# Optimization experiments

Hardware: AMD Instinct MI355X
Metric: run time of the kernel (lower is better)

Reference implementation:

```python
import jax, jax.numpy as jnp
import numpy as np

T, B, E, H = 1024, 4, 1024, 16
Dh = E // H
NEG_INF = float('-inf')


def setup_inputs() -> dict:
    key = jax.random.key(0)
    k1, k2, k3, k4 = jax.random.split(key, 4)
    return {
        'fwd_x': jax.random.normal(k1, (T, B, E), jnp.float32),
        'bwd_x': jax.random.normal(k2, (T, B, E), jnp.float32),
        'in_proj_weight': jax.random.normal(k3, (3 * E, E), jnp.float32) * 0.02,
        'in_proj_bias': jnp.zeros((3 * E,), jnp.float32),
        'out_w': jax.random.normal(k4, (E, E), jnp.float32) * 0.02,
        'out_b': jnp.zeros((E,), jnp.float32),
    }


def reference(fwd_x, bwd_x, in_proj_weight, in_proj_bias, out_w, out_b):
    t, b, e = fwd_x.shape
    s = 2 * t
    dtype = fwd_x.dtype
    zeros = jnp.zeros((1, b, e), dtype)
    # padded_fwd_x[0:t] -> [0, fwd_x[:-1]]; padded_bwd_x[1:t+1] -> [bwd_x[1:], 0]
    q_in = jnp.concatenate([zeros, fwd_x[:-1]], 0) + jnp.concatenate([bwd_x[1:], zeros], 0)
    kv = jnp.concatenate([fwd_x, bwd_x], 0)  # [s, b, e]

    wq, wk, wv = in_proj_weight[:e], in_proj_weight[e:2 * e], in_proj_weight[2 * e:]
    bq, bk, bv = in_proj_bias[:e], in_proj_bias[e:2 * e], in_proj_bias[2 * e:]
    q = (q_in @ wq.T + bq).reshape(t, b, H, Dh)
    k = (kv @ wk.T + bk).reshape(s, b, H, Dh)
    v = (kv @ wv.T + bv).reshape(s, b, H, Dh)

    # NOTE: original module never applies self.scaling in forward -- keep unscaled.
    attn_weights = jnp.einsum('tbhd,sbhd->bhts', q, k)  # [b, H, t, s]

    # mask_curr_state=True: allowed keys are j < i (fwd half) or j > i + t (bwd half)
    i = jnp.arange(t)[:, None]
    j = jnp.arange(s)[None, :]
    allowed = (j >= i + t + 1) | (j <= i - 1)
    mask_bias = jnp.where(allowed, 0.0, NEG_INF).astype(dtype)
    attn_weights = attn_weights + mask_bias[None, None]

    probs = jax.nn.softmax(attn_weights.astype(jnp.float32), axis=-1).astype(dtype)

    attn = jnp.einsum('bhts,sbhd->tbhd', probs, v).reshape(t, b, e)
    attn = attn @ out_w.T + out_b
    avg_weights = probs.mean(axis=1)  # [b, t, s]
    return attn, avg_weights
```

## Files before the change

### kernel.cpp

```cpp
#include <hip/hip_runtime.h>

typedef unsigned short u16;
typedef __attribute__((ext_vector_type(8))) short short8;
typedef __attribute__((ext_vector_type(4))) float f32x4;

#define SM_SHIFT2 34.6246800f
#if defined(__has_builtin)
#if __has_builtin(__builtin_amdgcn_exp2f)
#define EXP2(x) __builtin_amdgcn_exp2f(x)
#else
#define EXP2(x) __expf((x) * 0.6931471805599453f)
#endif
#else
#define EXP2(x) __expf((x) * 0.6931471805599453f)
#endif

__device__ __forceinline__ u16 f2b(float f) {
  unsigned u = __float_as_uint(f);
  unsigned r = (u + 0x7FFFu + ((u >> 16) & 1u)) >> 16;
  return (u16)r;
}

__device__ __forceinline__ void gload16(const u16* g, u16* l) {
  __builtin_amdgcn_global_load_lds((const __attribute__((address_space(1))) void*)g,
                                   (__attribute__((address_space(3))) void*)l, 16, 0, 0);
}

__device__ __forceinline__ void cast4(const float* __restrict__ src,
                                      u16* __restrict__ dst, int gid) {
  float4 v = *(const float4*)(src + (gid << 2));
  ushort4 o; o.x = f2b(v.x); o.y = f2b(v.y); o.z = f2b(v.z); o.w = f2b(v.w);
  *(ushort4*)(dst + (gid << 2)) = o;
}

__global__ __launch_bounds__(256) void prep_all(const float* __restrict__ fwd,
                                                const float* __restrict__ bwd,
                                                const float* __restrict__ w_in,
                                                const float* __restrict__ w_out,
                                                u16* __restrict__ qin,
                                                u16* __restrict__ kvf,
                                                u16* __restrict__ kvb,
                                                u16* __restrict__ wbf,
                                                u16* __restrict__ wobf,
                                                float* __restrict__ out_avg) {
  const int blk = blockIdx.x, tid = threadIdx.x;
  if (blk < 4096) {
    int gid = blk * 256 + tid;
    int n = gid >> 8;
    int e4 = (gid & 255) << 2;
    int t = n >> 2, b = n & 3;
    float4 acc = make_float4(0.f, 0.f, 0.f, 0.f);
    if (t > 0) {
      float4 v = *(const float4*)(fwd + (((t - 1) * 4 + b) << 10) + e4);
      acc.x += v.x; acc.y += v.y; acc.z += v.z; acc.w += v.w;
    }
    if (t < 1023) {
      float4 v = *(const float4*)(bwd + (((t + 1) * 4 + b) << 10) + e4);
      acc.x += v.x; acc.y += v.y; acc.z += v.z; acc.w += v.w;
    }
    ushort4 o; o.x = f2b(acc.x); o.y = f2b(acc.y); o.z = f2b(acc.z); o.w = f2b(acc.w);
    *(ushort4*)(qin + (n << 10) + e4) = o;
  } else if (blk < 8192) {
    cast4(fwd, kvf, (blk - 4096) * 256 + tid);
  } else if (blk < 12288) {
    cast4(bwd, kvb, (blk - 8192) * 256 + tid);
  } else if (blk < 15360) {
    cast4(w_in, wbf, (blk - 12288) * 256 + tid);
  } else if (blk < 16384) {
    cast4(w_out, wobf, (blk - 15360) * 256 + tid);
  } else {
    int z = blk - 16384;
    int mi = z % 15, bt2 = z / 15;
    int tb2 = bt2 & 15, b2 = bt2 >> 4;
    int s0z = (tb2 + 1 + mi) << 6, t0z = tb2 << 6;
    float* ob = out_avg + (size_t)b2 * 2097152 + (size_t)t0z * 2048 + s0z;
    float4 zz = make_float4(0.f, 0.f, 0.f, 0.f);
#pragma unroll
    for (int it = 0; it < 4; ++it) {
      int idx = it * 256 + tid;
      int rr = idx >> 4, c4 = (idx & 15) << 2;
      *(float4*)&ob[rr * 2048 + c4] = zz;
    }
  }
}

__global__ __launch_bounds__(512, 2) void gemm_kv256(const u16* __restrict__ A,
                                                     const u16* __restrict__ W,
                                                     const float* __restrict__ bias,
                                                     u16* __restrict__ outK,
                                                     u16* __restrict__ outV) {
  __shared__ u16 SH[65536];
  const int x = blockIdx.x & 7, local = blockIdx.x >> 3;
  const int mt = x * 4 + (local & 3);
  const int nt = local >> 2;
  const int m0 = mt << 8, n0 = nt << 8;
  const int tid = threadIdx.x;
  const int lane = tid & 63, wid = tid >> 6;
  const int wm = (wid >> 2) << 7;
  const int wn = (wid & 3) << 6;
  const int lr = lane & 15, lg = lane >> 4;
  const int scol = (lane & 7) << 3;
  const int swc = ((lane & 7) ^ (lane >> 3)) << 3;
  f32x4 acc[8][4] = {};
  auto At = [&](int buf) { return SH + buf * 16384; };
  auto Wt = [&](int buf) { return SH + 32768 + buf * 16384; };
  auto stage = [&](int buf, int k0) {
    u16* a = At(buf); u16* w = Wt(buf);
#pragma unroll
    for (int it = 0; it < 4; it++) {
      int row = (it * 8 + wid) * 8 + (lane >> 3);
      gload16(&A[(size_t)(m0 + row) * 1024 + k0 + swc], &a[row * 64 + scol]);
      gload16(&W[(size_t)(n0 + row) * 1024 + k0 + swc], &w[row * 64 + scol]);
    }
  };
  auto compute = [&](int buf) {
    const u16* a = At(buf); const u16* w = Wt(buf);
#pragma unroll
    for (int kk = 0; kk < 64; kk += 32) {
      int co = (((kk >> 3) + lg) ^ (lr & 7)) << 3;
      short8 af[8], bf[4];
#pragma unroll
      for (int i = 0; i < 8; i++)
        af[i] = *(const short8*)&a[(wm + i * 16 + lr) * 64 + co];
#pragma unroll
      for (int j = 0; j < 4; j++)
        bf[j] = *(const short8*)&w[(wn + j * 16 + lr) * 64 + co];
#pragma unroll
      for (int i = 0; i < 8; i++)
#pragma unroll
        for (int j = 0; j < 4; j++)
          acc[i][j] = __builtin_amdgcn_mfma_f32_16x16x32_bf16(af[i], bf[j], acc[i][j], 0, 0, 0);
    }
  };
  stage(0, 0);
  __syncthreads();
  for (int step = 0; step < 16; ++step) {
    const int cur = step & 1;
    if (step < 15) stage(cur ^ 1, (step + 1) << 6);
    compute(cur);
    __syncthreads();
  }
  u16* C = SH;
#pragma unroll
  for (int i = 0; i < 8; i++) {
#pragma unroll
    for (int j = 0; j < 4; j++) {
      int n = wn + j * 16 + lr;
      float bv = bias[n0 + n];
      int np = n ^ (lg << 4);
#pragma unroll
      for (int r = 0; r < 4; r++) {
        int m = wm + i * 16 + lg * 4 + r;
        C[m * 256 + np] = f2b(acc[i][j][r] + bv);
      }
    }
  }
  __syncthreads();
  const bool isK = (n0 < 1024);
  u16* ob = isK ? outK : outV;
  const int hbase = isK ? (n0 >> 6) : ((n0 - 1024) >> 6);
  const int ts0 = m0 >> 2;
  const int ts = tid >> 3, c8d = tid & 7;
#pragma unroll
  for (int k = 0; k < 16; ++k) {
    int tb = k >> 2, hh = k & 3;
    int m = ts * 4 + tb;
    int c8 = (hh * 8 + c8d) ^ ((ts & 3) << 1);
    uint4 val = *(const uint4*)&C[m * 256 + c8 * 8];
    size_t off = ((size_t)(tb * 16 + hbase + hh) * 2048 + ts0 + ts) * 64 + c8d * 8;
    *(uint4*)&ob[off] = val;
  }
}

template <int MODE, int MTX>
__global__ __launch_bounds__(256) void gemm_bt(const u16* __restrict__ A,
                                               const u16* __restrict__ W,
                                               const float* __restrict__ bias,
                                               void* __restrict__ outp) {
  __shared__ u16 At[2][128 * 64];
  __shared__ u16 Wt[2][128 * 64];
  const int x = blockIdx.x & 7, local = blockIdx.x >> 3;
  const int mt = x * MTX + (local % MTX);
  const int nt = local / MTX;
  const int m0 = mt << 7, n0 = nt << 7;
  const int tid = threadIdx.x;
  const int lane = tid & 63, wid = tid >> 6;
  const int wm = (wid >> 1) << 6, wn = (wid & 1) << 6;
  const int lr = lane & 15, lg = lane >> 4;
  const int srow = lane >> 3, scol = (lane & 7) << 3;
  const int swc = ((lane & 7) ^ srow) << 3;
  f32x4 acc[4][4] = {};
  auto stage = [&](int buf, int k0) {
#pragma unroll
    for (int it = 0; it < 4; it++) {
      int row = (it * 4 + wid) * 8 + srow;
      gload16(&A[(m0 + row) * 1024 + k0 + swc], &At[buf][row * 64 + scol]);
      gload16(&W[(n0 + row) * 1024 + k0 + swc], &Wt[buf][row * 64 + scol]);
    }
  };
  auto compute = [&](int buf) {
#pragma unroll
    for (int kk = 0; kk < 64; kk += 32) {
      short8 af[4], bf[4];
#pragma unroll
      for (int i = 0; i < 4; i++) {
        int co = (((kk >> 3) + lg) ^ (lr & 7)) << 3;
        af[i] = *(const short8*)&At[buf][(wm + i * 16 + lr) * 64 + co];
        bf[i] = *(const short8*)&Wt[buf][(wn + i * 16 + lr) * 64 + co];
      }
#pragma unroll
      for (int i = 0; i < 4; i++)
#pragma unroll
        for (int j = 0; j < 4; j++)
          acc[i][j] = __builtin_amdgcn_mfma_f32_16x16x32_bf16(af[i], bf[j], acc[i][j], 0, 0, 0);
    }
  };
  stage(0, 0);
  __syncthreads();
  for (int step = 0; step < 16; ++step) {
    const int cur = step & 1;
    if (step < 15) stage(cur ^ 1, (step + 1) << 6);
    compute(cur);
    __syncthreads();
  }
#pragma unroll
  for (int i = 0; i < 4; i++) {
#pragma unroll
    for (int j = 0; j < 4; j++) {
      int n = n0 + wn + j * 16 + lr;
      float bv = bias[n];
#pragma unroll
      for (int r = 0; r < 4; r++) {
        int m = m0 + wm + i * 16 + lg * 4 + r;
        float v = acc[i][j][r] + bv;
        if (MODE == 3) {
          ((float*)outp)[m * 1024 + n] = v;
        } else {
          v *= 1.44269504f;
          int tb = m & 3, ts = m >> 2, hh = n >> 6, d = n & 63;
          ((u16*)outp)[((tb * 16 + hh) * 1024 + ts) * 64 + d] = f2b(v);
        }
      }
    }
  }
}

__global__ __launch_bounds__(256) void transpose_v(const u16* __restrict__ v,
                                                   u16* __restrict__ vt) {
  __shared__ u16 L[64 * 66];
  const int blk = blockIdx.x;
  const int bh = blk >> 5, s0 = (blk & 31) << 6;
  const int tid = threadIdx.x;
  const u16* src = v + ((size_t)bh * 2048 + s0) * 64;
  u16* dst = vt + (size_t)bh * 64 * 2048 + s0;
#pragma unroll
  for (int it = 0; it < 2; ++it) {
    int idx = it * 256 + tid;
    int sl = idx >> 3, dc = (idx & 7) << 3;
    short8 v8 = *(const short8*)&src[sl * 64 + dc];
#pragma unroll
    for (int e = 0; e < 8; ++e)
      L[(dc + e) * 66 + sl] = (u16)v8[e];
  }
  __syncthreads();
#pragma unroll
  for (int it = 0; it < 2; ++it) {
    int idx = it * 256 + tid;
    int dr = idx >> 3, sc = (idx & 7) << 3;
    *(short8*)&dst[(size_t)dr * 2048 + sc] = *(const short8*)&L[dr * 66 + sc];
  }
}

__global__ __launch_bounds__(256) void attn_fwd(const u16* __restrict__ qb,
                                                const u16* __restrict__ kb,
                                                const u16* __restrict__ vtb,
                                                u16* __restrict__ attn_bf,
                                                float* __restrict__ st_il) {
  __shared__ u16 Kt[64 * 64];
  __shared__ u16 Vt[64 * 64];
  __shared__ u16 Pt[4][16 * 72];
  const int g = blockIdx.x;
  const int L = ((g & 7) << 7) | (g >> 3);
  const int t0 = (L & 15) << 6;
  const int h = (L >> 4) & 15;
  const int b = L >> 8;
  const int tid = threadIdx.x, lane = tid & 63, w = tid >> 6;
  const int lr = lane & 15, lg = lane >> 4;
  const int bh = b * 16 + h;
  const int sw0 = ((lg ^ (lr & 7)) << 3);
  const int sw1 = sw0 ^ 32;
  const u16* qrow = qb + ((bh << 10) + t0 + (w << 4) + lr) * 64;
  short8 qf0 = *(const short8*)&qrow[lg * 8];
  short8 qf1 = *(const short8*)&qrow[32 + lg * 8];
  const u16* kbase = kb + (size_t)(bh << 11) * 64;
  const u16* vbase = vtb + (size_t)(bh << 6) * 2048;
  f32x4 acc[4] = {};
  f32x4 accl = {};
  const int n1 = (t0 >> 6) + 1;
  const int grow = lane >> 3, gcol = (lane & 7) << 3;
  short8 ones;
#pragma unroll
  for (int j = 0; j < 8; ++j) ones[j] = (short)0x3F80;
  for (int ti = 0; ti < 17; ++ti) {
    const int s0 = (ti < n1) ? (ti << 6) : (t0 + 1024 + ((ti - n1) << 6));
    __syncthreads();
#pragma unroll
    for (int it = 0; it < 2; ++it) {
      int row = (it * 4 + w) * 8 + grow;
      int swc = (((lane & 7) ^ (row & 7)) << 3);
      gload16(&kbase[(size_t)(s0 + row) * 64 + swc], &Kt[row * 64 + gcol]);
      gload16(&vbase[(size_t)row * 2048 + s0 + swc], &Vt[row * 64 + gcol]);
    }
    __syncthreads();
    float pv[4][4];
    const bool maskt = (ti == n1 - 1) || (ti == n1);
    if (maskt) {
#pragma unroll
      for (int c = 0; c < 4; c++) {
        f32x4 sc = {};
        short8 kf0 = *(const short8*)&Kt[(c * 16 + lr) * 64 + sw0];
        short8 kf1 = *(const short8*)&Kt[(c * 16 + lr) * 64 + sw1];
        sc = __builtin_amdgcn_mfma_f32_16x16x32_bf16(qf0, kf0, sc, 0, 0, 0);
        sc = __builtin_amdgcn_mfma_f32_16x16x32_bf16(qf1, kf1, sc, 0, 0, 0);
        int j = s0 + c * 16 + lr;
#pragma unroll
        for (int r = 0; r < 4; r++) {
          int i = t0 + (w << 4) + lg * 4 + r;
          float e = EXP2(sc[r] - SM_SHIFT2);
          pv[c][r] = ((j < i) || (j > i + 1024)) ? e : 0.f;
        }
      }
    } else {
#pragma unroll
      for (int c = 0; c < 4; c++) {
        f32x4 sc = {};
        short8 kf0 = *(const short8*)&Kt[(c * 16 + lr) * 64 + sw0];
        short8 kf1 = *(const short8*)&Kt[(c * 16 + lr) * 64 + sw1];
        sc = __builtin_amdgcn_mfma_f32_16x16x32_bf16(qf0, kf0, sc, 0, 0, 0);
        sc = __builtin_amdgcn_mfma_f32_16x16x32_bf16(qf1, kf1, sc, 0, 0, 0);
#pragma unroll
        for (int r = 0; r < 4; r++)
          pv[c][r] = EXP2(sc[r] - SM_SHIFT2);
      }
    }
#pragma unroll
    for (int c = 0; c < 4; c++)
#pragma unroll
      for (int r = 0; r < 4; r++)
        Pt[w][(lg * 4 + r) * 72 + c * 16 + lr] = f2b(pv[c][r]);
    short8 pf0 = *(const short8*)&Pt[w][lr * 72 + lg * 8];
    short8 pf1 = *(const short8*)&Pt[w][lr * 72 + 32 + lg * 8];
    accl = __builtin_amdgcn_mfma_f32_16x16x32_bf16(pf0, ones, accl, 0, 0, 0);
    accl = __builtin_amdgcn_mfma_f32_16x16x32_bf16(pf1, ones, accl, 0, 0, 0);
#pragma unroll
    for (int dd = 0; dd < 4; dd++) {
      short8 vf0 = *(const short8*)&Vt[(dd * 16 + lr) * 64 + sw0];
      short8 vf1 = *(const short8*)&Vt[(dd * 16 + lr) * 64 + sw1];
      acc[dd] = __builtin_amdgcn_mfma_f32_16x16x32_bf16(pf0, vf0, acc[dd], 0, 0, 0);
      acc[dd] = __builtin_amdgcn_mfma_f32_16x16x32_bf16(pf1, vf1, acc[dd], 0, 0, 0);
    }
  }
  float inv[4];
#pragma unroll
  for (int r = 0; r < 4; r++) inv[r] = 1.f / accl[r];
  const int trow = t0 + (w << 4) + lg * 4;
#pragma unroll
  for (int dd = 0; dd < 4; dd++)
#pragma unroll
    for (int r = 0; r < 4; r++)
      attn_bf[((trow + r) * 4 + b) * 1024 + h * 64 + dd * 16 + lr] = f2b(acc[dd][r] * inv[r]);
#pragma unroll
  for (int r = 0; r < 4; r++)
    if (lr == r)
      st_il[(bh << 10) + trow + r] = inv[r];
}

__global__ __launch_bounds__(256) void attn_avg(const u16* __restrict__ qb,
                                                const u16* __restrict__ kb,
                                                const float* __restrict__ st_il,
                                                float* __restrict__ avg) {
  __shared__ u16 Kt[2][64 * 64];
  __shared__ float Si[16][64];
  const int g = blockIdx.x;
  const int L = (g & 7) * 136 + (g >> 3);
  const int l = L % 17;
  const int bt = L / 17;
  const int tb = bt & 15, b = bt >> 4;
  const int sb = (l <= tb) ? l : l + 15;
  const int s0 = sb << 6, t0 = tb << 6;
  const bool maskblk = (l == tb) || (l == tb + 1);
  const int tid = threadIdx.x, lane = tid & 63, w = tid >> 6;
  const int lr = lane & 15, lg = lane >> 4;
  const int trow = t0 + (w << 4) + lg * 4;
  float* obase = avg + (size_t)b * 2097152;
  for (int i = tid; i < 1024; i += 256) {
    int hh = i >> 6, tt = i & 63;
    Si[hh][tt] = st_il[(((b << 4) + hh) << 10) + t0 + tt];
  }
  const int sw0 = ((lg ^ (lr & 7)) << 3);
  const int sw1 = sw0 ^ 32;
  const int grow = lane >> 3, gcol = (lane & 7) << 3;
  const int srr = (w << 4) + lg * 4;
  auto stage = [&](int buf, int hh) {
    const u16* kb_h = kb + ((size_t)(((b << 4) + hh) << 11) + s0) * 64;
#pragma unroll
    for (int it = 0; it < 2; ++it) {
      int row = it * 32 + w * 8 + grow;
      int swc = (((lane & 7) ^ grow) << 3);
      gload16(&kb_h[(size_t)row * 64 + swc], &Kt[buf][row * 64 + gcol]);
    }
  };
  stage(0, 0);
  __syncthreads();
  float accv[4][4] = {};
  for (int h = 0; h < 16; h++) {
    const int cur = h & 1;
    if (h < 15) stage(cur ^ 1, h + 1);
    const int bh = (b << 4) + h;
    const u16* qrow = qb + ((bh << 10) + t0 + (w << 4) + lr) * 64;
    short8 qf0 = *(const short8*)&qrow[lg * 8];
    short8 qf1 = *(const short8*)&qrow[32 + lg * 8];
    float ih[4];
#pragma unroll
    for (int r = 0; r < 4; r++) ih[r] = Si[h][srr + r];
    if (maskblk) {
#pragma unroll
      for (int c = 0; c < 4; c++) {
        f32x4 sc = {};
        short8 kf0 = *(const short8*)&Kt[cur][(c * 16 + lr) * 64 + sw0];
        short8 kf1 = *(const short8*)&Kt[cur][(c * 16 + lr) * 64 + sw1];
        sc = __builtin_amdgcn_mfma_f32_16x16x32_bf16(qf0, kf0, sc, 0, 0, 0);
        sc = __builtin_amdgcn_mfma_f32_16x16x32_bf16(qf1, kf1, sc, 0, 0, 0);
        int j = s0 + c * 16 + lr;
#pragma unroll
        for (int r = 0; r < 4; r++) {
          int i = t0 + (w << 4) + lg * 4 + r;
          if ((j < i) || (j > i + 1024))
            accv[c][r] += EXP2(sc[r] - SM_SHIFT2) * ih[r];
        }
      }
    } else {
#pragma unroll
      for (int c = 0; c < 4; c++) {
        f32x4 sc = {};
        short8 kf0 = *(const short8*)&Kt[cur][(c * 16 + lr) * 64 + sw0];
        short8 kf1 = *(const short8*)&Kt[cur][(c * 16 + lr) * 64 + sw1];
        sc = __builtin_amdgcn_mfma_f32_16x16x32_bf16(qf0, kf0, sc, 0, 0, 0);
        sc = __builtin_amdgcn_mfma_f32_16x16x32_bf16(qf1, kf1, sc, 0, 0, 0);
#pragma unroll
        for (int r = 0; r < 4; r++)
          accv[c][r] += EXP2(sc[r] - SM_SHIFT2) * ih[r];
      }
    }
    __syncthreads();
  }
#pragma unroll
  for (int c = 0; c < 4; c++)
#pragma unroll
    for (int r = 0; r < 4; r++)
      obase[(trow + r) * 2048 + s0 + c * 16 + lr] = accv[c][r] * 0.0625f;
}

extern "C" void kernel_launch(void* const* d_in, const int* in_sizes, int n_in,
                              void* d_out, int out_size, void* d_ws, size_t ws_size,
                              hipStream_t stream) {
  const float* fwd   = (const float*)d_in[0];
  const float* bwd   = (const float*)d_in[1];
  const float* w_in  = (const float*)d_in[2];
  const float* b_in  = (const float*)d_in[3];
  const float* w_out = (const float*)d_in[4];
  const float* b_out = (const float*)d_in[5];

  char* ws = (char*)d_ws;
  u16*  q_in_bf = (u16*)(ws);
  u16*  kv_bf   = (u16*)(ws + 8388608);
  u16*  vt_bf   = (u16*)(ws + 8388608);
  u16*  w_bf    = (u16*)(ws + 25165824);
  u16*  wo_bf   = (u16*)(ws + 31457280);
  u16*  q_bf    = (u16*)(ws + 33554432);
  u16*  k_bf    = (u16*)(ws + 41943040);
  u16*  v_tmp   = (u16*)(ws + 58720256);
  u16*  attn_bf = (u16*)(ws + 75497472);
  float* st_il  = (float*)(ws + 83886080);

  float* out_attn = (float*)d_out;
  float* out_avg  = (float*)d_out + 4194304;

  prep_all<<<17344, 256, 0, stream>>>(fwd, bwd, w_in, w_out, q_in_bf, kv_bf,
                                      kv_bf + 4194304, w_bf, wo_bf, out_avg);

  gemm_bt<0, 4><<<256, 256, 0, stream>>>(q_in_bf, w_bf, b_in, (void*)q_bf);
  gemm_kv256<<<256, 512, 0, stream>>>(kv_bf, w_bf + 1048576, b_in + 1024,
                                      k_bf, v_tmp);
  transpose_v<<<2048, 256, 0, stream>>>(v_tmp, vt_bf);

  attn_fwd<<<1024, 256, 0, stream>>>(q_bf, k_bf, vt_bf, attn_bf, st_il);

  gemm_bt<3, 4><<<256, 256, 0, stream>>>(attn_bf, wo_bf, b_out,
                                         (void*)out_attn);

  attn_avg<<<1088, 256, 0, stream>>>(q_bf, k_bf, st_il, out_avg);
}
```

Measured before the change: 174.0 us.

## Interleave KV GEMM staging with MFMA in quarter-tile pieces using fine-grained waits

```diff
diff --git a/kernel.cpp b/kernel.cpp
--- a/kernel.cpp
+++ b/kernel.cpp
@@ -99,47 +99,62 @@
   const int wm = (wid >> 2) << 7;
   const int wn = (wid & 3) << 6;
   const int lr = lane & 15, lg = lane >> 4;
-  const int scol = (lane & 7) << 3;
-  const int swc = ((lane & 7) ^ (lane >> 3)) << 3;
+  const int co0 = ((lg ^ (lr & 7)) << 3);
+  const int co1 = (((4 + lg) ^ (lr & 7)) << 3);
+  const int rl = tid >> 3, ch = tid & 7;
+  const int ssw = ((ch ^ (rl & 7)) << 3);
+  const int arow = (rl & 31) + ((rl >> 5) << 7);
   f32x4 acc[8][4] = {};
   auto At = [&](int buf) { return SH + buf * 16384; };
   auto Wt = [&](int buf) { return SH + 32768 + buf * 16384; };
-  auto stage = [&](int buf, int k0) {
-    u16* a = At(buf); u16* w = Wt(buf);
-#pragma unroll
-    for (int it = 0; it < 4; it++) {
-      int row = (it * 8 + wid) * 8 + (lane >> 3);
-      gload16(&A[(size_t)(m0 + row) * 1024 + k0 + swc], &a[row * 64 + scol]);
-      gload16(&W[(size_t)(n0 + row) * 1024 + k0 + swc], &w[row * 64 + scol]);
-    }
+  auto stage_piece = [&](int buf, int k0, int q) {
+    int ar = (q << 5) + arow;
+    gload16(&A[(size_t)(m0 + ar) * 1024 + k0 + ssw], &At(buf)[ar * 64 + ch * 8]);
+    int wr = (q << 6) + rl;
+    gload16(&W[(size_t)(n0 + wr) * 1024 + k0 + ssw], &Wt(buf)[wr * 64 + ch * 8]);
   };
-  auto compute = [&](int buf) {
-    const u16* a = At(buf); const u16* w = Wt(buf);
-#pragma unroll
-    for (int kk = 0; kk < 64; kk += 32) {
-      int co = (((kk >> 3) + lg) ^ (lr & 7)) << 3;
-      short8 af[8], bf[4];
-#pragma unroll
-      for (int i = 0; i < 8; i++)
-        af[i] = *(const short8*)&a[(wm + i * 16 + lr) * 64 + co];
-#pragma unroll
-      for (int j = 0; j < 4; j++)
-        bf[j] = *(const short8*)&w[(wn + j * 16 + lr) * 64 + co];
-#pragma unroll
-      for (int i = 0; i < 8; i++)
-#pragma unroll
-        for (int j = 0; j < 4; j++)
-          acc[i][j] = __builtin_amdgcn_mfma_f32_16x16x32_bf16(af[i], bf[j], acc[i][j], 0, 0, 0);
-    }
-  };
-  stage(0, 0);
+#pragma unroll
+  for (int q = 0; q < 4; ++q) stage_piece(0, 0, q);
+  short8 wf[4][2];
+  for (int t = 0; t < 16; ++t) {
+    const int cur = t & 1;
+    const u16* a = At(cur);
+    const u16* w = Wt(cur);
+#pragma unroll
+    for (int q = 0; q < 4; ++q) {
+      if (q == 0) asm volatile("s_waitcnt vmcnt(0)" ::: "memory");
+      else        asm volatile("s_waitcnt vmcnt(6)" ::: "memory");
+      __builtin_amdgcn_s_barrier();
+      if (t < 15) stage_piece(cur ^ 1, (t + 1) << 6, q);
+      if (q == 0) {
+#pragma unroll
+        for (int j = 0; j < 4; ++j) {
+          int wrow = (wn + j * 16 + lr) * 64;
+          wf[j][0] = *(const short8*)&w[wrow + co0];
+          wf[j][1] = *(const short8*)&w[wrow + co1];
+        }
+      }
+      short8 af[2][2];
+#pragma unroll
+      for (int di = 0; di < 2; ++di) {
+        int row = (wm + (2 * q + di) * 16 + lr) * 64;
+        af[di][0] = *(const short8*)&a[row + co0];
+        af[di][1] = *(const short8*)&a[row + co1];
+      }
+      __builtin_amdgcn_s_setprio(1);
+#pragma unroll
+      for (int dk = 0; dk < 2; ++dk)
+#pragma unroll
+        for (int di = 0; di < 2; ++di)
+#pragma unroll
+          for (int j = 0; j < 4; ++j)
+            acc[2 * q + di][j] =
+                __builtin_amdgcn_mfma_f32_16x16x32_bf16(af[di][dk], wf[j][dk],
+                                                        acc[2 * q + di][j], 0, 0, 0);
+      __builtin_amdgcn_s_setprio(0);
+    }
+  }
   __syncthreads();
-  for (int step = 0; step < 16; ++step) {
-    const int cur = step & 1;
-    if (step < 15) stage(cur ^ 1, (step + 1) << 6);
-    compute(cur);
-    __syncthreads();
-  }
   u16* C = SH;
 #pragma unroll
   for (int i = 0; i < 8; i++) {
```

Result: no change. 175.5 us (+0.8%).
